# Performance work log

Measured on AMD Instinct MI355X. Metric: run time of the kernel, lower is better.

The kernel has to match this reference:

```python
import jax, jax.numpy as jnp
import numpy as np

TOP_K = 2
NUM_EXPERTS = 64
TEMPERATURE = 1.0

def setup_inputs() -> dict:
    key = jax.random.key(0)
    ks = jax.random.split(key, 4)
    B, L, D, DT, E = 4, 4096, 2048, 16, NUM_EXPERTS
    return {
        "x": jax.random.normal(ks[0], (B, L, D), dtype=jnp.float32),
        "z_task": jax.random.normal(ks[1], (B, DT), dtype=jnp.float32),
        "W_router": jax.random.normal(ks[2], (E, D + DT), dtype=jnp.float32) * 0.02,
        "W_task_proj": jax.random.normal(ks[3], (DT, DT), dtype=jnp.float32) * 0.25,
        "b_task_proj": jnp.zeros((DT,), dtype=jnp.float32),
        "expert_bias": jnp.zeros((E,), dtype=jnp.float32),
    }

def reference(x, z_task, W_router, W_task_proj, b_task_proj, expert_bias):
    B, L, D = x.shape
    E = W_router.shape[0]
    DT = z_task.shape[-1]
    # task_proj: Linear(d_task, d_task) + exact GELU
    tp = jax.nn.gelu(z_task @ W_task_proj.T + b_task_proj, approximate=False)  # [B, DT]
    # concat fusion: logits = [x ; task_proj] @ W_router^T, split to avoid materializing concat
    logits = (jnp.einsum('bld,ed->ble', x, W_router[:, :D])
              + jnp.einsum('bt,et->be', tp, W_router[:, D:])[:, None, :]
              + expert_bias)  # [B, L, E]
    probs = jax.nn.softmax(logits / TEMPERATURE, axis=-1)
    topw, topi = jax.lax.top_k(probs, TOP_K)  # [B, L, K]
    topw = topw / (topw.sum(axis=-1, keepdims=True) + 1e-8)
    # aux load-balance loss: E * sum_i f_i * P_i over flattened tokens
    mask = jax.nn.one_hot(topi, E, dtype=probs.dtype).sum(axis=-2) / TOP_K  # [B, L, E]
    f = mask.reshape(-1, E).mean(axis=0)
    P = probs.reshape(-1, E).mean(axis=0)
    aux_loss = E * (f * P).sum()
    return topw, topi, probs, aux_loss
```

## Files before the change

kernel.cpp:

```cpp
#include <hip/hip_runtime.h>
#include <math.h>


#define DDIM 2048
#define WROW 2064

typedef unsigned int u32;
typedef unsigned short u16;
typedef unsigned long long u64;
using short8 = __attribute__((ext_vector_type(8))) short;
using f32x4  = __attribute__((ext_vector_type(4))) float;
using u32x4  = __attribute__((ext_vector_type(4))) u32;

typedef const __attribute__((address_space(1))) u32* gp1;
typedef __attribute__((address_space(3))) u32* lp3;

#define BAR() do {                                                              \
        __builtin_amdgcn_s_barrier();                                           \
        asm volatile("" ::: "memory");                                          \
        __builtin_amdgcn_sched_barrier(0);                                      \
    } while (0)

__device__ __forceinline__ u16 bf16rne(float f) {
    u32 u = __float_as_uint(f);
    return (u16)((u + 0x7FFFu + ((u >> 16) & 1u)) >> 16);
}

__global__ void k01_prep(const float* __restrict__ Wr, u32* __restrict__ wh,
                         u32* __restrict__ wl, const float* __restrict__ z,
                         const float* __restrict__ Wp, const float* __restrict__ bp,
                         const float* __restrict__ eb, float* __restrict__ wsb) {
    const int t = threadIdx.x;
    if (blockIdx.x < 256) {
        const int g = blockIdx.x * 256 + t;
        const int e  = g >> 10;
        const int k  = (g & 1023) * 2;
        const int step = k >> 5, kb = (k >> 3) & 3, d = (k >> 1) & 3;
        const int grp = e >> 4, lane = kb * 16 + (e & 15);
        const float w0 = Wr[(size_t)e * WROW + k];
        const float w1 = Wr[(size_t)e * WROW + k + 1];
        const u16 h0 = bf16rne(w0);
        const u16 h1 = bf16rne(w1);
        const u16 l0 = bf16rne(w0 - __uint_as_float((u32)h0 << 16));
        const u16 l1 = bf16rne(w1 - __uint_as_float((u32)h1 << 16));
        const u32 oi = (u32)(((step * 4 + grp) * 64 + lane) * 4 + d);
        wh[oi] = ((u32)h1 << 16) | h0;
        wl[oi] = ((u32)l1 << 16) | l0;
    } else {
        __shared__ float tp[4][16];
        if (t < 64) {
            const int b = t >> 4, r = t & 15;
            float s = bp[r];
            #pragma unroll
            for (int i = 0; i < 16; ++i) s += z[b * 16 + i] * Wp[r * 16 + i];
            tp[b][r] = 0.5f * s * (1.0f + erff(s * 0.70710678118654752440f));
        }
        #pragma unroll
        for (int i = t; i < 1024; i += 256) wsb[256 + i] = 0.0f;
        __syncthreads();
        {
            const int b = t >> 6, e = t & 63;
            const float* wr = Wr + (size_t)e * WROW + DDIM;
            float s = eb[e];
            #pragma unroll
            for (int i = 0; i < 16; ++i) s += tp[b][i] * wr[i];
            wsb[b * 64 + e] = s;
        }
    }
}

__global__ __launch_bounds__(576, 1) void k2_mfma(const float* __restrict__ x,
                                                  const float* __restrict__ wsb,
                                                  const u32* __restrict__ whp,
                                                  const u32* __restrict__ wlp,
                                                  float* __restrict__ wacc,
                                                  float* __restrict__ out) {
    __shared__ __align__(16) u32 smem[17408];
    float* const lgf = (float*)smem;
    float* const pff = (float*)&smem[16384];

    const int tid   = threadIdx.x;
    const int wv    = __builtin_amdgcn_readfirstlane(tid >> 6);
    const int lane  = tid & 63;
    const int tok0b = blockIdx.x * 64;
    const int bb    = tok0b >> 12;

    if (wv == 8) {
#define BDMA(t, buf) do {                                                       \
            _Pragma("unroll")                                                   \
            for (int hl = 0; hl < 2; ++hl)                                      \
            _Pragma("unroll")                                                   \
            for (int hh = 0; hh < 2; ++hh)                                      \
            _Pragma("unroll")                                                   \
            for (int g = 0; g < 4; ++g) {                                       \
                const u32* _s = (hl ? wlp : whp) +                              \
                                ((t) + hh * 32) * 1024 + g * 256 + lane * 4;    \
                u32* _d = &smem[(buf) * 4096 + hl * 2048 + hh * 1024 + g * 256 + lane * 4];\
                __builtin_amdgcn_global_load_lds((gp1)_s, (lp3)_d, 16, 0, 0);   \
            }                                                                   \
        } while (0)
#define PSTEP(t, j) do {                                                        \
            BDMA((t) + 3, ((j) + 3) & 3);                                       \
            asm volatile("s_waitcnt vmcnt(32)" ::: "memory");                   \
            BAR();                                                              \
        } while (0)
        BDMA(0, 0); BDMA(1, 1); BDMA(2, 2);
        asm volatile("s_waitcnt vmcnt(32)" ::: "memory");
        BAR();
        for (int g7 = 0; g7 < 7; ++g7) {
            const int t0 = g7 * 4;
            PSTEP(t0 + 0, 0); PSTEP(t0 + 1, 1);
            PSTEP(t0 + 2, 2); PSTEP(t0 + 3, 3);
        }
        BDMA(31, 3);
        asm volatile("s_waitcnt vmcnt(32)" ::: "memory"); BAR();
        asm volatile("s_waitcnt vmcnt(16)" ::: "memory"); BAR();
        asm volatile("s_waitcnt vmcnt(0)"  ::: "memory"); BAR();
        BAR();
#undef BDMA
#undef PSTEP
    } else {
        const int tg  = wv & 3;
        const int h   = wv >> 2;
        const int row = lane & 15;
        const int kg  = lane >> 4;
        const int tok0 = tok0b + tg * 16;

        f32x4 acc[4];
        #pragma unroll
        for (int g = 0; g < 4; ++g) {
            const float tl = (h == 0) ? wsb[bb * 64 + g * 16 + row] : 0.0f;
            acc[g] = (f32x4){tl, tl, tl, tl};
        }
        #pragma unroll
        for (int g = 0; g < 4; ++g) asm volatile("" : "+v"(acc[g]));
        __builtin_amdgcn_sched_barrier(0);

        u64 xcur = (u64)(x + (size_t)(tok0 + row) * DDIM + h * 1024 + kg * 8);
        f32x4 xr[4][2];

#define SPLIT(xa, xb, Ah, Al) do {                                              \
            u32 h0_, h1_, h2_, h3_, l0_, l1_, l2_, l3_;                         \
            asm("v_cvt_pk_bf16_f32 %0, %1, %2" : "=v"(h0_) : "v"((xa)[0]), "v"((xa)[1])); \
            asm("v_cvt_pk_bf16_f32 %0, %1, %2" : "=v"(h1_) : "v"((xa)[2]), "v"((xa)[3])); \
            asm("v_cvt_pk_bf16_f32 %0, %1, %2" : "=v"(h2_) : "v"((xb)[0]), "v"((xb)[1])); \
            asm("v_cvt_pk_bf16_f32 %0, %1, %2" : "=v"(h3_) : "v"((xb)[2]), "v"((xb)[3])); \
            const float r0_ = (xa)[0] - __uint_as_float(h0_ << 16);             \
            const float r1_ = (xa)[1] - __uint_as_float(h0_ & 0xFFFF0000u);     \
            const float r2_ = (xa)[2] - __uint_as_float(h1_ << 16);             \
            const float r3_ = (xa)[3] - __uint_as_float(h1_ & 0xFFFF0000u);     \
            const float r4_ = (xb)[0] - __uint_as_float(h2_ << 16);             \
            const float r5_ = (xb)[1] - __uint_as_float(h2_ & 0xFFFF0000u);     \
            const float r6_ = (xb)[2] - __uint_as_float(h3_ << 16);             \
            const float r7_ = (xb)[3] - __uint_as_float(h3_ & 0xFFFF0000u);     \
            asm("v_cvt_pk_bf16_f32 %0, %1, %2" : "=v"(l0_) : "v"(r0_), "v"(r1_)); \
            asm("v_cvt_pk_bf16_f32 %0, %1, %2" : "=v"(l1_) : "v"(r2_), "v"(r3_)); \
            asm("v_cvt_pk_bf16_f32 %0, %1, %2" : "=v"(l2_) : "v"(r4_), "v"(r5_)); \
            asm("v_cvt_pk_bf16_f32 %0, %1, %2" : "=v"(l3_) : "v"(r6_), "v"(r7_)); \
            const u32x4 uh_ = {h0_, h1_, h2_, h3_};                             \
            const u32x4 ul_ = {l0_, l1_, l2_, l3_};                             \
            Ah = __builtin_bit_cast(short8, uh_);                               \
            Al = __builtin_bit_cast(short8, ul_);                               \
        } while (0)

#define MSTEP(xa, xb, BH, BL) do {                                              \
            short8 Ah, Al;                                                      \
            SPLIT(xa, xb, Ah, Al);                                              \
            _Pragma("unroll")                                                   \
            for (int g = 0; g < 4; ++g) {                                       \
                acc[g] = __builtin_amdgcn_mfma_f32_16x16x32_bf16(Ah, BH[g], acc[g], 0, 0, 0); \
                acc[g] = __builtin_amdgcn_mfma_f32_16x16x32_bf16(Ah, BL[g], acc[g], 0, 0, 0); \
                acc[g] = __builtin_amdgcn_mfma_f32_16x16x32_bf16(Al, BH[g], acc[g], 0, 0, 0); \
                acc[g] = __builtin_amdgcn_mfma_f32_16x16x32_bf16(Al, BL[g], acc[g], 0, 0, 0); \
            }                                                                   \
        } while (0)

#define CSTEP(j, WAITN, DOLOAD) do {                                            \
            short8 BH[4], BL[4];                                                \
            _Pragma("unroll")                                                   \
            for (int g2 = 0; g2 < 4; ++g2) {                                    \
                BH[g2] = *(const short8*)&smem[(j) * 4096 + h * 1024 + g2 * 256 + lane * 4]; \
                BL[g2] = *(const short8*)&smem[(j) * 4096 + 2048 + h * 1024 + g2 * 256 + lane * 4]; \
            }                                                                   \
            asm volatile("s_waitcnt vmcnt(" #WAITN ")"                          \
                : "+v"(xr[j][0]), "+v"(xr[j][1]));                              \
            __builtin_amdgcn_sched_barrier(0);                                  \
            MSTEP(xr[j][0], xr[j][1], BH, BL);                                  \
            if (DOLOAD) {                                                       \
                asm volatile("global_load_dwordx4 %0, %1, off offset:%c2"       \
                    : "=&v"(xr[j][0]) : "v"(xcur), "i"(((j) + 4) * 128));       \
                asm volatile("global_load_dwordx4 %0, %1, off offset:%c2"       \
                    : "=&v"(xr[j][1]) : "v"(xcur), "i"(((j) + 4) * 128 + 16));  \
            }                                                                   \
            BAR();                                                              \
        } while (0)

        #pragma unroll
        for (int j = 0; j < 4; ++j) {
            asm volatile("global_load_dwordx4 %0, %1, off offset:%c2"
                : "=&v"(xr[j][0]) : "v"(xcur), "i"(j * 128));
            asm volatile("global_load_dwordx4 %0, %1, off offset:%c2"
                : "=&v"(xr[j][1]) : "v"(xcur), "i"(j * 128 + 16));
        }
        BAR();
        for (int g7 = 0; g7 < 7; ++g7) {
            CSTEP(0, 6, 1); CSTEP(1, 6, 1); CSTEP(2, 6, 1); CSTEP(3, 6, 1);
            xcur += 512;
        }
        CSTEP(0, 6, 0); CSTEP(1, 4, 0); CSTEP(2, 2, 0); CSTEP(3, 0, 0);
#undef SPLIT
#undef MSTEP
#undef CSTEP

        #pragma unroll
        for (int g = 0; g < 4; ++g)
            #pragma unroll
            for (int r = 0; r < 4; ++r)
                lgf[h * 4352 + (tg * 16 + kg * 4 + r) * 68 + g * 16 + row] = acc[g][r];
    }

    __syncthreads();

    if (wv < 8) {
        float pacc = 0.0f, facc = 0.0f;
        for (int i = 0; i < 8; ++i) {
            const int tk = wv * 8 + i;
            const float v = lgf[tk * 68 + lane] + lgf[4352 + tk * 68 + lane];
            float m1 = v; int i1 = lane;
            #pragma unroll
            for (int off = 32; off; off >>= 1) {
                const float ov = __shfl_xor(m1, off, 64);
                const int   oi = __shfl_xor(i1, off, 64);
                if (ov > m1 || (ov == m1 && oi < i1)) { m1 = ov; i1 = oi; }
            }
            const float vx = (lane == i1) ? -3.4e38f : v;
            float m2 = vx; int i2 = lane;
            #pragma unroll
            for (int off = 32; off; off >>= 1) {
                const float ov = __shfl_xor(m2, off, 64);
                const int   oi = __shfl_xor(i2, off, 64);
                if (ov > m2 || (ov == m2 && oi < i2)) { m2 = ov; i2 = oi; }
            }
            const float p = __expf(v - m1);
            float s = p;
            #pragma unroll
            for (int off = 32; off; off >>= 1) s += __shfl_xor(s, off, 64);
            const float rZ = 1.0f / s;
            const float pn = p * rZ;
            const int   T  = tok0b + tk;
            out[65536 + (size_t)T * 64 + lane] = pn;
            pacc += pn;
            facc += (lane == i1 ? 1.0f : 0.0f) + (lane == i2 ? 1.0f : 0.0f);
            if (lane == 0) {
                const float q1 = rZ, q2 = __expf(m2 - m1) * rZ;
                const float dn = 1.0f / (q1 + q2 + 1e-8f);
                float2 tw; tw.x = q1 * dn; tw.y = q2 * dn;
                *(float2*)(out + (size_t)T * 2) = tw;
                float2 ti; ti.x = (float)i1; ti.y = (float)i2;
                *(float2*)(out + 32768 + (size_t)T * 2) = ti;
            }
        }
        pff[wv * 128 + lane]      = pacc;
        pff[wv * 128 + 64 + lane] = facc;
    }
    __syncthreads();

    if (wv == 0) {
        float ps = 0.0f, fs = 0.0f;
        #pragma unroll
        for (int w2 = 0; w2 < 8; ++w2) {
            ps += pff[w2 * 128 + lane];
            fs += pff[w2 * 128 + 64 + lane];
        }
        const int slot = blockIdx.x & 7;
        atomicAdd(wacc + slot * 128 + lane, ps);
        atomicAdd(wacc + slot * 128 + 64 + lane, fs);
    }
}

__global__ void k3_aux(const float* __restrict__ wsb, float* __restrict__ out) {
    const int e = threadIdx.x;
    float P = 0.0f, F = 0.0f;
    #pragma unroll
    for (int s = 0; s < 8; ++s) {
        P += wsb[256 + s * 128 + e];
        F += wsb[256 + s * 128 + 64 + e];
    }
    float val = P * F;
    #pragma unroll
    for (int off = 32; off; off >>= 1) val += __shfl_xor(val, off, 64);
    if (e == 0)
        out[1114112] = 64.0f * val / (16384.0f * 2.0f * 16384.0f);
}

extern "C" void kernel_launch(void* const* d_in, const int* in_sizes, int n_in,
                              void* d_out, int out_size, void* d_ws, size_t ws_size,
                              hipStream_t stream) {
    (void)in_sizes; (void)n_in; (void)out_size; (void)ws_size;
    const float* x  = (const float*)d_in[0];
    const float* z  = (const float*)d_in[1];
    const float* Wr = (const float*)d_in[2];
    const float* Wp = (const float*)d_in[3];
    const float* bp = (const float*)d_in[4];
    const float* eb = (const float*)d_in[5];
    float* out = (float*)d_out;
    float* wsb = (float*)d_ws;
    u32*   wfH = (u32*)(wsb + 1280);
    u32*   wfL = wfH + 65536;

    hipLaunchKernelGGL(k01_prep, dim3(257), dim3(256), 0, stream,
                       Wr, wfH, wfL, z, Wp, bp, eb, wsb);
    hipLaunchKernelGGL(k2_mfma,  dim3(256), dim3(576), 0, stream, x, wsb,
                       wfH, wfL, wsb + 256, out);
    hipLaunchKernelGGL(k3_aux,   dim3(1),   dim3(64),  0, stream, wsb, out);
}
```

Baseline: 46.04 us.

## Switch router GEMM to 32x32x16 MFMA with fewer, larger compute waves

Replaces the 16x16x32 bf16 MFMA tiling (8 compute waves, 16 tokens each) with 32x32x16 MFMA tiles (4 compute waves, 32 tokens by 64 experts each). The weight prepack layout, the LDS DMA pattern, the x prefetch depth and the logits writeback are all reorganised to match. The aim is fewer B-fragment LDS reads per FLOP and higher MFMA efficiency. In exchange there are fewer waves per CU to hide latency, more accumulator and x registers per wave, and a heavier softmax/top-k epilogue per wave.

```diff
diff --git a/kernel.cpp b/kernel.cpp
--- a/kernel.cpp
+++ b/kernel.cpp
@@ -9,6 +9,7 @@
 typedef unsigned short u16;
 typedef unsigned long long u64;
 using short8 = __attribute__((ext_vector_type(8))) short;
+using f32x16 = __attribute__((ext_vector_type(16))) float;
 using f32x4  = __attribute__((ext_vector_type(4))) float;
 using u32x4  = __attribute__((ext_vector_type(4))) u32;
 
@@ -32,20 +33,21 @@
                          const float* __restrict__ eb, float* __restrict__ wsb) {
     const int t = threadIdx.x;
     if (blockIdx.x < 256) {
-        const int g = blockIdx.x * 256 + t;
-        const int e  = g >> 10;
-        const int k  = (g & 1023) * 2;
-        const int step = k >> 5, kb = (k >> 3) & 3, d = (k >> 1) & 3;
-        const int grp = e >> 4, lane = kb * 16 + (e & 15);
+        const int g    = blockIdx.x * 256 + t;
+        const int d    = g & 3;
+        const int lane = (g >> 2) & 63;
+        const int egrp = (g >> 8) & 1;
+        const int s16  = g >> 9;
+        const int k = s16 * 16 + ((lane >> 5) << 3) + d * 2;
+        const int e = egrp * 32 + (lane & 31);
         const float w0 = Wr[(size_t)e * WROW + k];
         const float w1 = Wr[(size_t)e * WROW + k + 1];
         const u16 h0 = bf16rne(w0);
         const u16 h1 = bf16rne(w1);
         const u16 l0 = bf16rne(w0 - __uint_as_float((u32)h0 << 16));
         const u16 l1 = bf16rne(w1 - __uint_as_float((u32)h1 << 16));
-        const u32 oi = (u32)(((step * 4 + grp) * 64 + lane) * 4 + d);
-        wh[oi] = ((u32)h1 << 16) | h0;
-        wl[oi] = ((u32)l1 << 16) | l0;
+        wh[g] = ((u32)h1 << 16) | h0;
+        wl[g] = ((u32)l1 << 16) | l0;
     } else {
         __shared__ float tp[4][16];
         if (t < 64) {
@@ -69,13 +71,13 @@
     }
 }
 
-__global__ __launch_bounds__(576, 1) void k2_mfma(const float* __restrict__ x,
+__global__ __launch_bounds__(320, 1) void k2_mfma(const float* __restrict__ x,
                                                   const float* __restrict__ wsb,
                                                   const u32* __restrict__ whp,
                                                   const u32* __restrict__ wlp,
                                                   float* __restrict__ wacc,
                                                   float* __restrict__ out) {
-    __shared__ __align__(16) u32 smem[17408];
+    __shared__ __align__(16) u32 smem[16896];
     float* const lgf = (float*)smem;
     float* const pff = (float*)&smem[16384];
 
@@ -85,17 +87,20 @@
     const int tok0b = blockIdx.x * 64;
     const int bb    = tok0b >> 12;
 
-    if (wv == 8) {
+    if (wv == 4) {
 #define BDMA(t, buf) do {                                                       \
             _Pragma("unroll")                                                   \
-            for (int hl = 0; hl < 2; ++hl)                                      \
-            _Pragma("unroll")                                                   \
-            for (int hh = 0; hh < 2; ++hh)                                      \
-            _Pragma("unroll")                                                   \
-            for (int g = 0; g < 4; ++g) {                                       \
-                const u32* _s = (hl ? wlp : whp) +                              \
-                                ((t) + hh * 32) * 1024 + g * 256 + lane * 4;    \
-                u32* _d = &smem[(buf) * 4096 + hl * 2048 + hh * 1024 + g * 256 + lane * 4];\
+            for (int h2 = 0; h2 < 2; ++h2)                                      \
+            _Pragma("unroll")                                                   \
+            for (int kk = 0; kk < 2; ++kk)                                      \
+            _Pragma("unroll")                                                   \
+            for (int eg = 0; eg < 2; ++eg)                                      \
+            _Pragma("unroll")                                                   \
+            for (int hl = 0; hl < 2; ++hl) {                                    \
+                const int s16 = h2 * 64 + 2 * (t) + kk;                         \
+                const u32* _s = (hl ? wlp : whp) + (s16 * 2 + eg) * 256 + lane * 4; \
+                u32* _d = &smem[(buf) * 4096 + h2 * 2048 + kk * 1024 +          \
+                                eg * 512 + hl * 256 + lane * 4];                \
                 __builtin_amdgcn_global_load_lds((gp1)_s, (lp3)_d, 16, 0, 0);   \
             }                                                                   \
         } while (0)
@@ -120,24 +125,25 @@
 #undef BDMA
 #undef PSTEP
     } else {
-        const int tg  = wv & 3;
-        const int h   = wv >> 2;
-        const int row = lane & 15;
-        const int kg  = lane >> 4;
-        const int tok0 = tok0b + tg * 16;
-
-        f32x4 acc[4];
-        #pragma unroll
-        for (int g = 0; g < 4; ++g) {
-            const float tl = (h == 0) ? wsb[bb * 64 + g * 16 + row] : 0.0f;
-            acc[g] = (f32x4){tl, tl, tl, tl};
-        }
-        #pragma unroll
-        for (int g = 0; g < 4; ++g) asm volatile("" : "+v"(acc[g]));
+        const int tg  = wv & 1;
+        const int h   = wv >> 1;
+        const int row = lane & 31;
+        const int kq  = lane >> 5;
+        const int tok0 = tok0b + tg * 32;
+
+        f32x16 acc[2];
+        #pragma unroll
+        for (int eg = 0; eg < 2; ++eg) {
+            const float tl = (h == 0) ? wsb[bb * 64 + eg * 32 + (lane & 31)] : 0.0f;
+            #pragma unroll
+            for (int r = 0; r < 16; ++r) acc[eg][r] = tl;
+        }
+        #pragma unroll
+        for (int eg = 0; eg < 2; ++eg) asm volatile("" : "+v"(acc[eg]));
         __builtin_amdgcn_sched_barrier(0);
 
-        u64 xcur = (u64)(x + (size_t)(tok0 + row) * DDIM + h * 1024 + kg * 8);
-        f32x4 xr[4][2];
+        u64 xcur = (u64)(x + (size_t)(tok0 + row) * DDIM + h * 1024 + kq * 8);
+        f32x4 xr[4][4];
 
 #define SPLIT(xa, xb, Ah, Al) do {                                              \
             u32 h0_, h1_, h2_, h3_, l0_, l1_, l2_, l3_;                         \
@@ -163,34 +169,41 @@
             Al = __builtin_bit_cast(short8, ul_);                               \
         } while (0)
 
-#define MSTEP(xa, xb, BH, BL) do {                                              \
-            short8 Ah, Al;                                                      \
-            SPLIT(xa, xb, Ah, Al);                                              \
-            _Pragma("unroll")                                                   \
-            for (int g = 0; g < 4; ++g) {                                       \
-                acc[g] = __builtin_amdgcn_mfma_f32_16x16x32_bf16(Ah, BH[g], acc[g], 0, 0, 0); \
-                acc[g] = __builtin_amdgcn_mfma_f32_16x16x32_bf16(Ah, BL[g], acc[g], 0, 0, 0); \
-                acc[g] = __builtin_amdgcn_mfma_f32_16x16x32_bf16(Al, BH[g], acc[g], 0, 0, 0); \
-                acc[g] = __builtin_amdgcn_mfma_f32_16x16x32_bf16(Al, BL[g], acc[g], 0, 0, 0); \
-            }                                                                   \
-        } while (0)
-
 #define CSTEP(j, WAITN, DOLOAD) do {                                            \
-            short8 BH[4], BL[4];                                                \
-            _Pragma("unroll")                                                   \
-            for (int g2 = 0; g2 < 4; ++g2) {                                    \
-                BH[g2] = *(const short8*)&smem[(j) * 4096 + h * 1024 + g2 * 256 + lane * 4]; \
-                BL[g2] = *(const short8*)&smem[(j) * 4096 + 2048 + h * 1024 + g2 * 256 + lane * 4]; \
+            short8 BH[2][2], BL[2][2];                                          \
+            _Pragma("unroll")                                                   \
+            for (int kk = 0; kk < 2; ++kk)                                      \
+            _Pragma("unroll")                                                   \
+            for (int eg = 0; eg < 2; ++eg) {                                    \
+                BH[kk][eg] = *(const short8*)&smem[(j) * 4096 + h * 2048 +      \
+                                kk * 1024 + eg * 512 + lane * 4];               \
+                BL[kk][eg] = *(const short8*)&smem[(j) * 4096 + h * 2048 +      \
+                                kk * 1024 + eg * 512 + 256 + lane * 4];         \
             }                                                                   \
             asm volatile("s_waitcnt vmcnt(" #WAITN ")"                          \
-                : "+v"(xr[j][0]), "+v"(xr[j][1]));                              \
+                : "+v"(xr[j][0]), "+v"(xr[j][1]), "+v"(xr[j][2]), "+v"(xr[j][3]));\
             __builtin_amdgcn_sched_barrier(0);                                  \
-            MSTEP(xr[j][0], xr[j][1], BH, BL);                                  \
+            _Pragma("unroll")                                                   \
+            for (int kk = 0; kk < 2; ++kk) {                                    \
+                short8 Ah, Al;                                                  \
+                SPLIT(xr[j][2 * kk], xr[j][2 * kk + 1], Ah, Al);                \
+                _Pragma("unroll")                                               \
+                for (int eg = 0; eg < 2; ++eg) {                                \
+                    acc[eg] = __builtin_amdgcn_mfma_f32_32x32x16_bf16(Ah, BH[kk][eg], acc[eg], 0, 0, 0); \
+                    acc[eg] = __builtin_amdgcn_mfma_f32_32x32x16_bf16(Ah, BL[kk][eg], acc[eg], 0, 0, 0); \
+                    acc[eg] = __builtin_amdgcn_mfma_f32_32x32x16_bf16(Al, BH[kk][eg], acc[eg], 0, 0, 0); \
+                    acc[eg] = __builtin_amdgcn_mfma_f32_32x32x16_bf16(Al, BL[kk][eg], acc[eg], 0, 0, 0); \
+                }                                                               \
+            }                                                                   \
             if (DOLOAD) {                                                       \
                 asm volatile("global_load_dwordx4 %0, %1, off offset:%c2"       \
                     : "=&v"(xr[j][0]) : "v"(xcur), "i"(((j) + 4) * 128));       \
                 asm volatile("global_load_dwordx4 %0, %1, off offset:%c2"       \
                     : "=&v"(xr[j][1]) : "v"(xcur), "i"(((j) + 4) * 128 + 16));  \
+                asm volatile("global_load_dwordx4 %0, %1, off offset:%c2"       \
+                    : "=&v"(xr[j][2]) : "v"(xcur), "i"(((j) + 4) * 128 + 64));  \
+                asm volatile("global_load_dwordx4 %0, %1, off offset:%c2"       \
+                    : "=&v"(xr[j][3]) : "v"(xcur), "i"(((j) + 4) * 128 + 80));  \
             }                                                                   \
             BAR();                                                              \
         } while (0)
@@ -201,30 +214,35 @@
                 : "=&v"(xr[j][0]) : "v"(xcur), "i"(j * 128));
             asm volatile("global_load_dwordx4 %0, %1, off offset:%c2"
                 : "=&v"(xr[j][1]) : "v"(xcur), "i"(j * 128 + 16));
+            asm volatile("global_load_dwordx4 %0, %1, off offset:%c2"
+                : "=&v"(xr[j][2]) : "v"(xcur), "i"(j * 128 + 64));
+            asm volatile("global_load_dwordx4 %0, %1, off offset:%c2"
+                : "=&v"(xr[j][3]) : "v"(xcur), "i"(j * 128 + 80));
         }
         BAR();
         for (int g7 = 0; g7 < 7; ++g7) {
-            CSTEP(0, 6, 1); CSTEP(1, 6, 1); CSTEP(2, 6, 1); CSTEP(3, 6, 1);
+            CSTEP(0, 12, 1); CSTEP(1, 12, 1); CSTEP(2, 12, 1); CSTEP(3, 12, 1);
             xcur += 512;
         }
-        CSTEP(0, 6, 0); CSTEP(1, 4, 0); CSTEP(2, 2, 0); CSTEP(3, 0, 0);
+        CSTEP(0, 12, 0); CSTEP(1, 8, 0); CSTEP(2, 4, 0); CSTEP(3, 0, 0);
 #undef SPLIT
-#undef MSTEP
 #undef CSTEP
 
         #pragma unroll
-        for (int g = 0; g < 4; ++g)
-            #pragma unroll
-            for (int r = 0; r < 4; ++r)
-                lgf[h * 4352 + (tg * 16 + kg * 4 + r) * 68 + g * 16 + row] = acc[g][r];
+        for (int eg = 0; eg < 2; ++eg)
+            #pragma unroll
+            for (int r = 0; r < 16; ++r) {
+                const int trow = (r & 3) + 8 * (r >> 2) + 4 * kq;
+                lgf[h * 4352 + (tg * 32 + trow) * 68 + eg * 32 + (lane & 31)] = acc[eg][r];
+            }
     }
 
     __syncthreads();
 
-    if (wv < 8) {
+    if (wv < 4) {
         float pacc = 0.0f, facc = 0.0f;
-        for (int i = 0; i < 8; ++i) {
-            const int tk = wv * 8 + i;
+        for (int i = 0; i < 16; ++i) {
+            const int tk = wv * 16 + i;
             const float v = lgf[tk * 68 + lane] + lgf[4352 + tk * 68 + lane];
             float m1 = v; int i1 = lane;
             #pragma unroll
@@ -268,7 +286,7 @@
     if (wv == 0) {
         float ps = 0.0f, fs = 0.0f;
         #pragma unroll
-        for (int w2 = 0; w2 < 8; ++w2) {
+        for (int w2 = 0; w2 < 4; ++w2) {
             ps += pff[w2 * 128 + lane];
             fs += pff[w2 * 128 + 64 + lane];
         }
@@ -310,7 +328,7 @@
 
     hipLaunchKernelGGL(k01_prep, dim3(257), dim3(256), 0, stream,
                        Wr, wfH, wfL, z, Wp, bp, eb, wsb);
-    hipLaunchKernelGGL(k2_mfma,  dim3(256), dim3(576), 0, stream, x, wsb,
+    hipLaunchKernelGGL(k2_mfma,  dim3(256), dim3(320), 0, stream, x, wsb,
                        wfH, wfL, wsb + 256, out);
     hipLaunchKernelGGL(k3_aux,   dim3(1),   dim3(64),  0, stream, wsb, out);
 }
```

After: 57.03 us. 23.9% more time.

## Deepen weight LDS ring to eight stages and barrier every two k-steps

Applied to the files above, without the earlier changes.

Doubles the shared-memory weight ring from four to eight slices, so the producer wave issues two DMA slices per epoch. Consumer waves now sync once per two k-steps instead of every step, and the register ring for x is indexed modulo four. The aim is to halve block-wide barrier count and keep more weight prefetch in flight. In exchange, LDS use roughly doubles to about 132 KB per block, and the new producer/consumer schedule must stay consistent with the buffer indexing and offsets.

```diff
diff --git a/kernel.cpp b/kernel.cpp
--- a/kernel.cpp
+++ b/kernel.cpp
@@ -75,9 +75,9 @@
                                                   const u32* __restrict__ wlp,
                                                   float* __restrict__ wacc,
                                                   float* __restrict__ out) {
-    __shared__ __align__(16) u32 smem[17408];
+    __shared__ __align__(16) u32 smem[33792];
     float* const lgf = (float*)smem;
-    float* const pff = (float*)&smem[16384];
+    float* const pff = (float*)&smem[32768];
 
     const int tid   = threadIdx.x;
     const int wv    = __builtin_amdgcn_readfirstlane(tid >> 6);
@@ -86,7 +86,7 @@
     const int bb    = tok0b >> 12;
 
     if (wv == 8) {
-#define BDMA(t, buf) do {                                                       \
+#define BDMA(tb, buf) do {                                                      \
             _Pragma("unroll")                                                   \
             for (int hl = 0; hl < 2; ++hl)                                      \
             _Pragma("unroll")                                                   \
@@ -94,31 +94,31 @@
             _Pragma("unroll")                                                   \
             for (int g = 0; g < 4; ++g) {                                       \
                 const u32* _s = (hl ? wlp : whp) +                              \
-                                ((t) + hh * 32) * 1024 + g * 256 + lane * 4;    \
+                                ((tb) + hh * 32) * 1024 + g * 256 + lane * 4;   \
                 u32* _d = &smem[(buf) * 4096 + hl * 2048 + hh * 1024 + g * 256 + lane * 4];\
                 __builtin_amdgcn_global_load_lds((gp1)_s, (lp3)_d, 16, 0, 0);   \
             }                                                                   \
         } while (0)
-#define PSTEP(t, j) do {                                                        \
-            BDMA((t) + 3, ((j) + 3) & 3);                                       \
+        BDMA(0, 0); BDMA(1, 1); BDMA(2, 2);
+        asm volatile("s_waitcnt vmcnt(16)" ::: "memory");
+        BAR();
+        BDMA(3, 3);
+        int tb = 4;
+#define PEPOCH(b0, b1) do {                                                     \
+            BDMA(tb, b0); BDMA(tb + 1, b1); tb += 2;                            \
             asm volatile("s_waitcnt vmcnt(32)" ::: "memory");                   \
             BAR();                                                              \
         } while (0)
-        BDMA(0, 0); BDMA(1, 1); BDMA(2, 2);
-        asm volatile("s_waitcnt vmcnt(32)" ::: "memory");
+        for (int p = 0; p < 3; ++p) {
+            PEPOCH(4, 5); PEPOCH(6, 7);
+            PEPOCH(0, 1); PEPOCH(2, 3);
+        }
+        PEPOCH(4, 5); PEPOCH(6, 7);
+        asm volatile("s_waitcnt vmcnt(0)" ::: "memory");
         BAR();
-        for (int g7 = 0; g7 < 7; ++g7) {
-            const int t0 = g7 * 4;
-            PSTEP(t0 + 0, 0); PSTEP(t0 + 1, 1);
-            PSTEP(t0 + 2, 2); PSTEP(t0 + 3, 3);
-        }
-        BDMA(31, 3);
-        asm volatile("s_waitcnt vmcnt(32)" ::: "memory"); BAR();
-        asm volatile("s_waitcnt vmcnt(16)" ::: "memory"); BAR();
-        asm volatile("s_waitcnt vmcnt(0)"  ::: "memory"); BAR();
         BAR();
 #undef BDMA
-#undef PSTEP
+#undef PEPOCH
     } else {
         const int tg  = wv & 3;
         const int h   = wv >> 2;
@@ -183,16 +183,15 @@
                 BL[g2] = *(const short8*)&smem[(j) * 4096 + 2048 + h * 1024 + g2 * 256 + lane * 4]; \
             }                                                                   \
             asm volatile("s_waitcnt vmcnt(" #WAITN ")"                          \
-                : "+v"(xr[j][0]), "+v"(xr[j][1]));                              \
+                : "+v"(xr[(j) & 3][0]), "+v"(xr[(j) & 3][1]));                  \
             __builtin_amdgcn_sched_barrier(0);                                  \
-            MSTEP(xr[j][0], xr[j][1], BH, BL);                                  \
+            MSTEP(xr[(j) & 3][0], xr[(j) & 3][1], BH, BL);                      \
             if (DOLOAD) {                                                       \
                 asm volatile("global_load_dwordx4 %0, %1, off offset:%c2"       \
-                    : "=&v"(xr[j][0]) : "v"(xcur), "i"(((j) + 4) * 128));       \
+                    : "=&v"(xr[(j) & 3][0]) : "v"(xcur), "i"(((j) + 4) * 128)); \
                 asm volatile("global_load_dwordx4 %0, %1, off offset:%c2"       \
-                    : "=&v"(xr[j][1]) : "v"(xcur), "i"(((j) + 4) * 128 + 16));  \
+                    : "=&v"(xr[(j) & 3][1]) : "v"(xcur), "i"(((j) + 4) * 128 + 16)); \
             }                                                                   \
-            BAR();                                                              \
         } while (0)
 
         #pragma unroll
@@ -203,11 +202,17 @@
                 : "=&v"(xr[j][1]) : "v"(xcur), "i"(j * 128 + 16));
         }
         BAR();
-        for (int g7 = 0; g7 < 7; ++g7) {
-            CSTEP(0, 6, 1); CSTEP(1, 6, 1); CSTEP(2, 6, 1); CSTEP(3, 6, 1);
-            xcur += 512;
-        }
-        CSTEP(0, 6, 0); CSTEP(1, 4, 0); CSTEP(2, 2, 0); CSTEP(3, 0, 0);
+        for (int it = 0; it < 3; ++it) {
+            CSTEP(0, 6, 1); CSTEP(1, 6, 1); BAR();
+            CSTEP(2, 6, 1); CSTEP(3, 6, 1); BAR();
+            CSTEP(4, 6, 1); CSTEP(5, 6, 1); BAR();
+            CSTEP(6, 6, 1); CSTEP(7, 6, 1); BAR();
+            xcur += 1024;
+        }
+        CSTEP(0, 6, 1); CSTEP(1, 6, 1); BAR();
+        CSTEP(2, 6, 1); CSTEP(3, 6, 1); BAR();
+        CSTEP(4, 6, 0); CSTEP(5, 4, 0); BAR();
+        CSTEP(6, 2, 0); CSTEP(7, 0, 0); BAR();
 #undef SPLIT
 #undef MSTEP
 #undef CSTEP
```

After: 46.49 us. Within noise of the previous version (+1.0%).
